# Performance work log

Hardware: AMD Instinct MI355X
Metric: run time of the kernel (lower is better)

## Reference

```python
import jax, jax.numpy as jnp
import numpy as np

N = 16384      # total nodes
SEQ = 512      # nodes per graph
NG = 32        # graphs (N = NG*SEQ)
D = 128        # dim_h
H = 8          # heads
E = 262144     # edges
BN_EPS = 1e-5


def _bn(x, g, b):
    # BatchNorm1d, training-mode stats over the node axis (biased var, as torch)
    mu = x.mean(axis=0)
    var = x.var(axis=0)
    return (x - mu) * jax.lax.rsqrt(var + BN_EPS) * g + b


def setup_inputs() -> dict:
    key = jax.random.key(0)
    ks = jax.random.split(key, 24)
    w = lambda k, shp: (jax.random.normal(k, shp, jnp.float32) * 0.05)
    x = jax.random.normal(ks[0], (N, D), jnp.float32)
    # within-graph edges: dst in same graph as src
    src = jax.random.randint(ks[1], (E,), 0, N, dtype=jnp.int32)
    dst = (src // SEQ) * SEQ + jax.random.randint(ks[2], (E,), 0, SEQ, dtype=jnp.int32)
    edge_index = jnp.stack([src, dst])
    edge_attr = jax.random.normal(ks[3], (E, D), jnp.float32)
    return {
        'x': x, 'edge_index': edge_index, 'edge_attr': edge_attr,
        'gin_w1': w(ks[4], (D, D)), 'gin_b1': jnp.zeros((D,), jnp.float32),
        'gin_w2': w(ks[5], (D, D)), 'gin_b2': jnp.zeros((D,), jnp.float32),
        'bn1l_g': jnp.ones((D,), jnp.float32), 'bn1l_b': jnp.zeros((D,), jnp.float32),
        'in_proj_w': w(ks[6], (3 * D, D)), 'in_proj_b': jnp.zeros((3 * D,), jnp.float32),
        'out_proj_w': w(ks[7], (D, D)), 'out_proj_b': jnp.zeros((D,), jnp.float32),
        'bn1a_g': jnp.ones((D,), jnp.float32), 'bn1a_b': jnp.zeros((D,), jnp.float32),
        'ff_w1': w(ks[8], (D, 2 * D)), 'ff_b1': jnp.zeros((2 * D,), jnp.float32),
        'ff_w2': w(ks[9], (2 * D, D)), 'ff_b2': jnp.zeros((D,), jnp.float32),
        'bn2_g': jnp.ones((D,), jnp.float32), 'bn2_b': jnp.zeros((D,), jnp.float32),
    }


def reference(x, edge_index, edge_attr, gin_w1, gin_b1, gin_w2, gin_b2,
              bn1l_g, bn1l_b, in_proj_w, in_proj_b, out_proj_w, out_proj_b,
              bn1a_g, bn1a_b, ff_w1, ff_b1, ff_w2, ff_b2, bn2_g, bn2_b):
    h_in1 = x
    src, dst = edge_index[0], edge_index[1]
    # --- local GINE: aggr_i = sum_{j->i} relu(x_j + e_ji); nn((1+eps)*x + aggr), eps=0
    msg = jax.nn.relu(x[src] + edge_attr)                 # [E, D]
    aggr = jax.ops.segment_sum(msg, dst, num_segments=N)  # [N, D]
    z = x + aggr
    h_local = jax.nn.relu(z @ gin_w1 + gin_b1) @ gin_w2 + gin_b2
    h_local = h_in1 + h_local                # residual (dropout=0)
    h_local = _bn(h_local, bn1l_g, bn1l_b)
    # --- global Transformer attention over dense batch (equal-size graphs => reshape)
    hd = x.reshape(NG, SEQ, D)
    qkv = hd @ in_proj_w.T + in_proj_b       # [NG, SEQ, 3D]
    q, k, v = jnp.split(qkv, 3, axis=-1)
    dh = D // H
    q = q.reshape(NG, SEQ, H, dh)
    k = k.reshape(NG, SEQ, H, dh)
    v = v.reshape(NG, SEQ, H, dh)
    scores = jnp.einsum('bqhd,bkhd->bhqk', q, k) / jnp.sqrt(jnp.float32(dh))
    attn = jax.nn.softmax(scores, axis=-1)
    o = jnp.einsum('bhqk,bkhd->bqhd', attn, v).reshape(NG, SEQ, D)
    h_attn = (o @ out_proj_w.T + out_proj_b).reshape(N, D)
    h_attn = h_in1 + h_attn                  # residual (attn_dropout=0)
    h_attn = _bn(h_attn, bn1a_g, bn1a_b)
    # --- combine + FFN block
    h = h_local + h_attn
    ff = jax.nn.relu(h @ ff_w1 + ff_b1) @ ff_w2 + ff_b2
    h = h + ff
    h = _bn(h, bn2_g, bn2_b)
    return h
```

## Files before the change

kernel.cpp:

```cpp
#include <hip/hip_runtime.h>


#define N_NODES 16384
#define SEQL    512
#define NGRAPH  32
#define DIM     128
#define NHEAD   8
#define DHEAD   16
#define NEDGE   262144

typedef __bf16 bf16;
typedef __bf16 bf16x8 __attribute__((ext_vector_type(8)));
typedef __bf16 bf16x4 __attribute__((ext_vector_type(4)));
typedef float  f32x4  __attribute__((ext_vector_type(4)));

__device__ inline f32x4 mfma16(bf16x8 a, bf16x8 b, f32x4 c) {
  return __builtin_amdgcn_mfma_f32_16x16x32_bf16(a, b, c, 0, 0, 0);
}

__global__ __launch_bounds__(256) void prep_k(
    const float* __restrict__ gw1, const float* __restrict__ gw2,
    const float* __restrict__ ipw, const float* __restrict__ opw,
    const float* __restrict__ fw1, const float* __restrict__ fw2,
    bf16* __restrict__ W, int* __restrict__ cnt, float* __restrict__ stats)
{
  int i = blockIdx.x * 256 + threadIdx.x;
  if (i < 16384) {
    W[i] = (bf16)gw1[(i & 127) * 128 + (i >> 7)];
  } else if (i < 32768) {
    int j = i - 16384;
    W[i] = (bf16)gw2[(j & 127) * 128 + (j >> 7)];
  } else if (i < 81920) {
    W[i] = (bf16)ipw[i - 32768];
  } else if (i < 98304) {
    W[i] = (bf16)opw[i - 81920];
  } else if (i < 131072) {
    int j = i - 98304;
    W[i] = (bf16)fw1[(j & 127) * 256 + (j >> 7)];
  } else if (i < 163840) {
    int j = i - 131072;
    W[i] = (bf16)fw2[(j & 255) * 128 + (j >> 8)];
  } else if (i < 163840 + 16384) {
    cnt[i - 163840] = 0;
  } else if (i < 163840 + 16384 + 768) {
    stats[i - 163840 - 16384] = 0.f;
  }
}

__global__ __launch_bounds__(256) void edge_count_k(const int* __restrict__ ei,
                                                    int* __restrict__ cnt)
{
  int e = blockIdx.x * 256 + threadIdx.x;
  if (e < NEDGE) atomicAdd(&cnt[ei[NEDGE + e]], 1);
}

__global__ __launch_bounds__(1024) void scan_k(const int* __restrict__ cnt,
                                               int* __restrict__ off,
                                               int* __restrict__ cur)
{
  __shared__ int part[1024];
  int t = threadIdx.x;
  int base = t * 16;
  int v[16];
  int s = 0;
#pragma unroll
  for (int j = 0; j < 16; ++j) { v[j] = s; s += cnt[base + j]; }
  part[t] = s;
  __syncthreads();
  for (int d = 1; d < 1024; d <<= 1) {
    int y = (t >= d) ? part[t - d] : 0;
    __syncthreads();
    part[t] += y;
    __syncthreads();
  }
  int bo = (t > 0) ? part[t - 1] : 0;
#pragma unroll
  for (int j = 0; j < 16; ++j) {
    int o = bo + v[j];
    off[base + j] = o;
    cur[base + j] = o;
  }
  if (t == 1023) off[16384] = bo + s;
}

__global__ __launch_bounds__(256) void edge_scatter_k(const int* __restrict__ ei,
                                                      int* __restrict__ cur,
                                                      int2* __restrict__ se)
{
  int e = blockIdx.x * 256 + threadIdx.x;
  if (e < NEDGE) {
    int s = ei[e];
    int d = ei[NEDGE + e];
    int p = atomicAdd(&cur[d], 1);
    se[p] = make_int2(s, e);
  }
}

__global__ __launch_bounds__(256) void aggr_k(
    const float* __restrict__ x, const float* __restrict__ ea,
    const int* __restrict__ off, const int2* __restrict__ se,
    float* __restrict__ z)
{
  int node = blockIdx.x * 4 + (threadIdx.x >> 6);
  int lane = threadIdx.x & 63;
  int c = lane * 2;
  int o0 = off[node], o1 = off[node + 1];
  float a0 = 0.f, a1 = 0.f;
  int j = o0;
  for (; j + 4 <= o1; j += 4) {
    int2 p0 = se[j], p1 = se[j + 1], p2 = se[j + 2], p3 = se[j + 3];
    float2 x0 = *(const float2*)(x + (size_t)p0.x * 128 + c);
    float2 e0 = *(const float2*)(ea + (size_t)p0.y * 128 + c);
    float2 x1 = *(const float2*)(x + (size_t)p1.x * 128 + c);
    float2 e1 = *(const float2*)(ea + (size_t)p1.y * 128 + c);
    float2 x2 = *(const float2*)(x + (size_t)p2.x * 128 + c);
    float2 e2 = *(const float2*)(ea + (size_t)p2.y * 128 + c);
    float2 x3 = *(const float2*)(x + (size_t)p3.x * 128 + c);
    float2 e3 = *(const float2*)(ea + (size_t)p3.y * 128 + c);
    a0 += fmaxf(x0.x + e0.x, 0.f) + fmaxf(x1.x + e1.x, 0.f) +
          fmaxf(x2.x + e2.x, 0.f) + fmaxf(x3.x + e3.x, 0.f);
    a1 += fmaxf(x0.y + e0.y, 0.f) + fmaxf(x1.y + e1.y, 0.f) +
          fmaxf(x2.y + e2.y, 0.f) + fmaxf(x3.y + e3.y, 0.f);
  }
  for (; j < o1; ++j) {
    int2 p = se[j];
    float2 xe = *(const float2*)(x + (size_t)p.x * 128 + c);
    float2 ae = *(const float2*)(ea + (size_t)p.y * 128 + c);
    a0 += fmaxf(xe.x + ae.x, 0.f);
    a1 += fmaxf(xe.y + ae.y, 0.f);
  }
  float2 xn = *(const float2*)(x + (size_t)node * 128 + c);
  *(float2*)(z + (size_t)node * 128 + c) = make_float2(xn.x + a0, xn.y + a1);
}

template <int NCH, int KCH, bool RELU, int RESID, bool STATS, int OUTMODE>
__global__ __launch_bounds__(256) void gemm_k(
    const float* __restrict__ Aptr, const bf16* __restrict__ Wt,
    const float* __restrict__ bias, const float* __restrict__ resid,
    float* __restrict__ outF, bf16* __restrict__ oq, bf16* __restrict__ okk,
    bf16* __restrict__ ov, float* __restrict__ stats)
{
  constexpr int KIN = KCH * 128;
  constexpr int NLD = NCH * 128;
  __shared__ bf16 Alds[32][136];
  __shared__ bf16 Wlds[128][136];
  __shared__ float slds[256];
  int tid = threadIdx.x;
  int wave = tid >> 6, lane = tid & 63, quad = lane >> 4, l16 = lane & 15;
  int rg = wave >> 1, chalf = wave & 1;
  int m0 = blockIdx.x * 32;
  if (STATS) slds[tid] = 0.f;

  for (int nc = 0; nc < NCH; ++nc) {
    f32x4 acc[4];
#pragma unroll
    for (int t = 0; t < 4; ++t) acc[t] = (f32x4){0.f, 0.f, 0.f, 0.f};
    for (int kc = 0; kc < KCH; ++kc) {
      if (!(nc == 0 && kc == 0)) __syncthreads();
      if (nc == 0 || KCH > 1) {
        int r = tid >> 3, c16 = (tid & 7) * 16;
        const float* src = Aptr + (size_t)(m0 + r) * KIN + kc * 128 + c16;
        float4 v0 = *(const float4*)(src);
        float4 v1 = *(const float4*)(src + 4);
        float4 v2 = *(const float4*)(src + 8);
        float4 v3 = *(const float4*)(src + 12);
        *(bf16x8*)&Alds[r][c16] =
            (bf16x8){(bf16)v0.x, (bf16)v0.y, (bf16)v0.z, (bf16)v0.w,
                     (bf16)v1.x, (bf16)v1.y, (bf16)v1.z, (bf16)v1.w};
        *(bf16x8*)&Alds[r][c16 + 8] =
            (bf16x8){(bf16)v2.x, (bf16)v2.y, (bf16)v2.z, (bf16)v2.w,
                     (bf16)v3.x, (bf16)v3.y, (bf16)v3.z, (bf16)v3.w};
      }
      {
        int n = tid >> 1, ch = (tid & 1) * 64;
        const bf16* src = Wt + (size_t)(nc * 128 + n) * KIN + kc * 128 + ch;
        bf16* dst = &Wlds[n][ch];
#pragma unroll
        for (int j = 0; j < 8; ++j)
          *(bf16x8*)(dst + j * 8) = *(const bf16x8*)(src + j * 8);
      }
      __syncthreads();
#pragma unroll
      for (int kt = 0; kt < 4; ++kt) {
        bf16x8 af = *(const bf16x8*)&Alds[rg * 16 + l16][kt * 32 + quad * 8];
#pragma unroll
        for (int nt = 0; nt < 4; ++nt) {
          bf16x8 bfr =
              *(const bf16x8*)&Wlds[chalf * 64 + nt * 16 + l16][kt * 32 + quad * 8];
          acc[nt] = mfma16(af, bfr, acc[nt]);
        }
      }
    }
    int rowb = m0 + rg * 16 + quad * 4;
#pragma unroll
    for (int nt = 0; nt < 4; ++nt) {
      int n = chalf * 64 + nt * 16 + l16;
      int gcol = nc * 128 + n;
      float bv = bias[gcol];
      float vals[4];
#pragma unroll
      for (int r = 0; r < 4; ++r) {
        float v = acc[nt][r] + bv;
        if (RELU) v = fmaxf(v, 0.f);
        if (RESID) v += resid[(size_t)(rowb + r) * 128 + n];
        vals[r] = v;
        if (OUTMODE == 0) {
          outF[(size_t)(rowb + r) * NLD + gcol] = v;
        } else {
          bf16* ob = (nc == 0) ? oq : ((nc == 1) ? okk : ov);
          ob[(size_t)(rowb + r) * 128 + n] = (bf16)v;
        }
      }
      if (STATS) {
        float s = vals[0] + vals[1] + vals[2] + vals[3];
        float q2 = vals[0] * vals[0] + vals[1] * vals[1] +
                   vals[2] * vals[2] + vals[3] * vals[3];
        s += __shfl_xor(s, 16);  s += __shfl_xor(s, 32);
        q2 += __shfl_xor(q2, 16); q2 += __shfl_xor(q2, 32);
        if (quad == 0) {
          atomicAdd(&slds[n * 2], s);
          atomicAdd(&slds[n * 2 + 1], q2);
        }
      }
    }
  }
  if (STATS) {
    __syncthreads();
    if (tid < 128) {
      atomicAdd(&stats[tid], slds[tid * 2]);
      atomicAdd(&stats[128 + tid], slds[tid * 2 + 1]);
    }
  }
}

__global__ __launch_bounds__(256) void attn_k(
    const bf16* __restrict__ qg, const bf16* __restrict__ kg,
    const bf16* __restrict__ vg, float* __restrict__ og)
{
  __shared__ bf16 Klds[512][16];
  __shared__ bf16 Vlds[16][520];
  __shared__ bf16 Plds[4][16][136];
  int b = blockIdx.x;
  int half = b & 1, hh = (b >> 1) & 7, g = b >> 4;
  int tid = threadIdx.x;
  const size_t gbase = (size_t)g * 512 * 128 + hh * 16;
  for (int r = tid; r < 512; r += 256) {
    const bf16* src = kg + gbase + (size_t)r * 128;
    *(bf16x8*)&Klds[r][0] = *(const bf16x8*)src;
    *(bf16x8*)&Klds[r][8] = *(const bf16x8*)(src + 8);
  }
  for (int r = tid; r < 512; r += 256) {
    const bf16* src = vg + gbase + (size_t)r * 128;
#pragma unroll
    for (int d = 0; d < 16; ++d) Vlds[d][r] = src[d];
  }
  __syncthreads();
  int wave = tid >> 6, lane = tid & 63, quad = lane >> 4, l16 = lane & 15;
  const bf16x8 z8 = {};
  for (int it = 0; it < 4; ++it) {
    int qt = half * 16 + it * 4 + wave;
    bf16x8 qf = z8;
    if (quad < 2)
      qf = *(const bf16x8*)(qg + gbase + (size_t)(qt * 16 + l16) * 128 + quad * 8);
    f32x4 S[32];
#pragma unroll
    for (int jt = 0; jt < 32; ++jt) {
      bf16x8 kf = z8;
      if (quad < 2) kf = *(const bf16x8*)&Klds[jt * 16 + l16][quad * 8];
      S[jt] = mfma16(kf, qf, (f32x4){0.f, 0.f, 0.f, 0.f});
    }
    float mx = -1e30f;
#pragma unroll
    for (int jt = 0; jt < 32; ++jt)
#pragma unroll
      for (int r = 0; r < 4; ++r) mx = fmaxf(mx, S[jt][r]);
    mx = fmaxf(mx, __shfl_xor(mx, 16));
    mx = fmaxf(mx, __shfl_xor(mx, 32));
    float sm = 0.f;
#pragma unroll
    for (int jt = 0; jt < 32; ++jt)
#pragma unroll
      for (int r = 0; r < 4; ++r) {
        float e = __expf((S[jt][r] - mx) * 0.25f);
        S[jt][r] = e;
        sm += e;
      }
    sm += __shfl_xor(sm, 16);
    sm += __shfl_xor(sm, 32);
    float rinv = 1.f / sm;
    f32x4 O = (f32x4){0.f, 0.f, 0.f, 0.f};
#pragma unroll
    for (int qd = 0; qd < 4; ++qd) {
#pragma unroll
      for (int jt2 = 0; jt2 < 8; ++jt2)
#pragma unroll
        for (int r = 0; r < 4; ++r)
          Plds[wave][l16][jt2 * 16 + quad * 4 + r] =
              (bf16)(S[qd * 8 + jt2][r] * rinv);
#pragma unroll
      for (int kt = 0; kt < 4; ++kt) {
        bf16x8 pf = *(const bf16x8*)&Plds[wave][l16][kt * 32 + quad * 8];
        bf16x8 vf = *(const bf16x8*)&Vlds[l16][qd * 128 + kt * 32 + quad * 8];
        O = mfma16(vf, pf, O);
      }
    }
    *(float4*)(og + (size_t)(g * 512 + qt * 16 + l16) * 128 + hh * 16 + quad * 4) =
        make_float4(O[0], O[1], O[2], O[3]);
  }
}

__global__ __launch_bounds__(256) void combine_k(
    const float* __restrict__ hl, const float* __restrict__ ha,
    const float* __restrict__ stats,
    const float* __restrict__ g1, const float* __restrict__ b1,
    const float* __restrict__ g2, const float* __restrict__ b2,
    float* __restrict__ h)
{
  __shared__ float sc1[128], sh1[128], sc2[128], sh2[128];
  int tid = threadIdx.x;
  if (tid < 128) {
    const float inv = 1.f / 16384.f;
    float mu = stats[tid] * inv;
    float var = stats[128 + tid] * inv - mu * mu;
    float s = g1[tid] * rsqrtf(var + 1e-5f);
    sc1[tid] = s; sh1[tid] = b1[tid] - mu * s;
    mu = stats[256 + tid] * inv;
    var = stats[384 + tid] * inv - mu * mu;
    s = g2[tid] * rsqrtf(var + 1e-5f);
    sc2[tid] = s; sh2[tid] = b2[tid] - mu * s;
  }
  __syncthreads();
  size_t i = ((size_t)blockIdx.x * 256 + tid) * 4;
  int c = (int)(i & 127);
  float4 a = *(const float4*)(hl + i);
  float4 bb = *(const float4*)(ha + i);
  float4 o;
  o.x = a.x * sc1[c] + sh1[c] + bb.x * sc2[c] + sh2[c];
  o.y = a.y * sc1[c + 1] + sh1[c + 1] + bb.y * sc2[c + 1] + sh2[c + 1];
  o.z = a.z * sc1[c + 2] + sh1[c + 2] + bb.z * sc2[c + 2] + sh2[c + 2];
  o.w = a.w * sc1[c + 3] + sh1[c + 3] + bb.w * sc2[c + 3] + sh2[c + 3];
  *(float4*)(h + i) = o;
}

__global__ __launch_bounds__(256) void apply_k(
    const float* __restrict__ h2, const float* __restrict__ stats,
    const float* __restrict__ g, const float* __restrict__ b,
    float* __restrict__ out)
{
  __shared__ float sc[128], sh[128];
  int tid = threadIdx.x;
  if (tid < 128) {
    const float inv = 1.f / 16384.f;
    float mu = stats[512 + tid] * inv;
    float var = stats[640 + tid] * inv - mu * mu;
    float s = g[tid] * rsqrtf(var + 1e-5f);
    sc[tid] = s; sh[tid] = b[tid] - mu * s;
  }
  __syncthreads();
  size_t i = ((size_t)blockIdx.x * 256 + tid) * 4;
  int c = (int)(i & 127);
  float4 a = *(const float4*)(h2 + i);
  float4 o;
  o.x = a.x * sc[c] + sh[c];
  o.y = a.y * sc[c + 1] + sh[c + 1];
  o.z = a.z * sc[c + 2] + sh[c + 2];
  o.w = a.w * sc[c + 3] + sh[c + 3];
  *(float4*)(out + i) = o;
}

extern "C" void kernel_launch(void* const* d_in, const int* in_sizes, int n_in,
                              void* d_out, int out_size, void* d_ws, size_t ws_size,
                              hipStream_t stream)
{
  (void)in_sizes; (void)n_in; (void)out_size; (void)ws_size;
  const float* x      = (const float*)d_in[0];
  const int*   ei     = (const int*)d_in[1];
  const float* ea     = (const float*)d_in[2];
  const float* gw1    = (const float*)d_in[3];
  const float* gb1    = (const float*)d_in[4];
  const float* gw2    = (const float*)d_in[5];
  const float* gb2    = (const float*)d_in[6];
  const float* bn1l_g = (const float*)d_in[7];
  const float* bn1l_b = (const float*)d_in[8];
  const float* ipw    = (const float*)d_in[9];
  const float* ipb    = (const float*)d_in[10];
  const float* opw    = (const float*)d_in[11];
  const float* opb    = (const float*)d_in[12];
  const float* bn1a_g = (const float*)d_in[13];
  const float* bn1a_b = (const float*)d_in[14];
  const float* fw1    = (const float*)d_in[15];
  const float* fb1    = (const float*)d_in[16];
  const float* fw2    = (const float*)d_in[17];
  const float* fb2    = (const float*)d_in[18];
  const float* bn2_g  = (const float*)d_in[19];
  const float* bn2_b  = (const float*)d_in[20];

  char* ws = (char*)d_ws;
  const size_t KB = 1024, MB = 1048576;
  bf16*  W     = (bf16*)(ws + 0);
  float* stats = (float*)(ws + 320 * KB);
  int*   cnt   = (int*)(ws + 384 * KB);
  int*   off   = (int*)(ws + 448 * KB);
  int*   cur   = (int*)(ws + 576 * KB);
  int2*  se    = (int2*)(ws + 640 * KB);
  float* z   = (float*)(ws + 3 * MB);
  float* hl  = (float*)(ws + 11 * MB);
  bf16*  qb  = (bf16*)(ws + 19 * MB);
  bf16*  kb  = (bf16*)(ws + 23 * MB);
  bf16*  vb  = (bf16*)(ws + 27 * MB);
  float* ob  = (float*)(ws + 31 * MB);
  float* ha  = (float*)(ws + 39 * MB);
  float* hb  = (float*)(ws + 47 * MB);
  float* t1  = (float*)qb;
  float* ff1 = z;
  float* h2  = ob;
  float* out = (float*)d_out;

  prep_k<<<708, 256, 0, stream>>>(gw1, gw2, ipw, opw, fw1, fw2, W, cnt, stats);
  edge_count_k<<<1024, 256, 0, stream>>>(ei, cnt);
  scan_k<<<1, 1024, 0, stream>>>(cnt, off, cur);
  edge_scatter_k<<<1024, 256, 0, stream>>>(ei, cur, se);
  aggr_k<<<4096, 256, 0, stream>>>(x, ea, off, se, z);
  gemm_k<1, 1, true, 0, false, 0><<<512, 256, 0, stream>>>(
      z, W + 0, gb1, nullptr, t1, nullptr, nullptr, nullptr, nullptr);
  gemm_k<1, 1, false, 1, true, 0><<<512, 256, 0, stream>>>(
      t1, W + 16384, gb2, x, hl, nullptr, nullptr, nullptr, stats + 0);
  gemm_k<3, 1, false, 0, false, 1><<<512, 256, 0, stream>>>(
      x, W + 32768, ipb, nullptr, nullptr, qb, kb, vb, nullptr);
  attn_k<<<512, 256, 0, stream>>>(qb, kb, vb, ob);
  gemm_k<1, 1, false, 1, true, 0><<<512, 256, 0, stream>>>(
      ob, W + 81920, opb, x, ha, nullptr, nullptr, nullptr, stats + 256);
  combine_k<<<2048, 256, 0, stream>>>(hl, ha, stats, bn1l_g, bn1l_b, bn1a_g, bn1a_b, hb);
  gemm_k<2, 1, true, 0, false, 0><<<512, 256, 0, stream>>>(
      hb, W + 98304, fb1, nullptr, ff1, nullptr, nullptr, nullptr, nullptr);
  gemm_k<1, 2, false, 1, true, 0><<<512, 256, 0, stream>>>(
      ff1, W + 131072, fb2, hb, h2, nullptr, nullptr, nullptr, stats + 512);
  apply_k<<<2048, 256, 0, stream>>>(h2, stats, bn2_g, bn2_b, out);
}
```

Before: 428.8 us.

## Fuse entire pipeline into one cooperative persistent megakernel with grid syncs

Replaces the chain of separate launches (weight prep, edge count, scan, scatter, aggregation, GEMMs, attention, BN combine, apply) with a single cooperative kernel that uses grid.sync between phases. The two GIN GEMMs and the QKV projection are fused per row tile, keeping intermediates in shared memory, and the scan is parallelised across blocks. The aim is to remove launch overhead and intermediate global round-trips. In exchange it adds grid-wide barriers, caps occupancy at the cooperative grid size, and puts heavy pressure on shared memory.

```diff
diff --git a/kernel.cpp b/kernel.cpp
--- a/kernel.cpp
+++ b/kernel.cpp
@@ -1,371 +1,494 @@
 #include <hip/hip_runtime.h>
-
-
-#define N_NODES 16384
-#define SEQL    512
-#define NGRAPH  32
-#define DIM     128
-#define NHEAD   8
-#define DHEAD   16
-#define NEDGE   262144
+#include <hip/hip_cooperative_groups.h>
+
+namespace cg = cooperative_groups;
+
+
+#define NNODES 16384
+#define NEDGE  262144
 
 typedef __bf16 bf16;
 typedef __bf16 bf16x8 __attribute__((ext_vector_type(8)));
-typedef __bf16 bf16x4 __attribute__((ext_vector_type(4)));
 typedef float  f32x4  __attribute__((ext_vector_type(4)));
 
 __device__ inline f32x4 mfma16(bf16x8 a, bf16x8 b, f32x4 c) {
   return __builtin_amdgcn_mfma_f32_16x16x32_bf16(a, b, c, 0, 0, 0);
 }
 
-__global__ __launch_bounds__(256) void prep_k(
-    const float* __restrict__ gw1, const float* __restrict__ gw2,
-    const float* __restrict__ ipw, const float* __restrict__ opw,
-    const float* __restrict__ fw1, const float* __restrict__ fw2,
-    bf16* __restrict__ W, int* __restrict__ cnt, float* __restrict__ stats)
-{
-  int i = blockIdx.x * 256 + threadIdx.x;
-  if (i < 16384) {
-    W[i] = (bf16)gw1[(i & 127) * 128 + (i >> 7)];
-  } else if (i < 32768) {
-    int j = i - 16384;
-    W[i] = (bf16)gw2[(j & 127) * 128 + (j >> 7)];
-  } else if (i < 81920) {
-    W[i] = (bf16)ipw[i - 32768];
-  } else if (i < 98304) {
-    W[i] = (bf16)opw[i - 81920];
-  } else if (i < 131072) {
-    int j = i - 98304;
-    W[i] = (bf16)fw1[(j & 127) * 256 + (j >> 7)];
-  } else if (i < 163840) {
-    int j = i - 131072;
-    W[i] = (bf16)fw2[(j & 255) * 128 + (j >> 8)];
-  } else if (i < 163840 + 16384) {
-    cnt[i - 163840] = 0;
-  } else if (i < 163840 + 16384 + 768) {
-    stats[i - 163840 - 16384] = 0.f;
-  }
+struct PK {
+  const float *x, *ea; const int* ei;
+  const float *gw1, *gb1, *gw2, *gb2;
+  const float *bn1l_g, *bn1l_b;
+  const float *ipw, *ipb, *opw, *opb;
+  const float *bn1a_g, *bn1a_b;
+  const float *fw1, *fb1, *fw2, *fb2;
+  const float *bn2_g, *bn2_b;
+  bf16* W; float* stats; int *cnt, *off, *cur, *psum; int2* se;
+  float *z, *hl, *ob, *ha, *h2, *out;
+  bf16 *qb, *kb, *vb;
+};
+
+#define SMEM_BYTES 79872
+
+__device__ inline void load_w(const bf16* __restrict__ src, int ks,
+                              bf16* __restrict__ Wl, int tid) {
+  int n = tid >> 1, c = (tid & 1) * 64;
+  const bf16* s = src + (size_t)n * ks + c;
+  bf16* d = Wl + n * 136 + c;
+#pragma unroll
+  for (int j = 0; j < 8; ++j)
+    *(bf16x8*)(d + j * 8) = *(const bf16x8*)(s + j * 8);
 }
 
-__global__ __launch_bounds__(256) void edge_count_k(const int* __restrict__ ei,
-                                                    int* __restrict__ cnt)
-{
-  int e = blockIdx.x * 256 + threadIdx.x;
-  if (e < NEDGE) atomicAdd(&cnt[ei[NEDGE + e]], 1);
+__device__ inline void load_a32(const float* __restrict__ src,
+                                bf16* __restrict__ Al, int tid) {
+  int r = tid >> 3, c = (tid & 7) * 16;
+  const float* s = src + (size_t)r * 128 + c;
+  float4 v0 = *(const float4*)s, v1 = *(const float4*)(s + 4);
+  float4 v2 = *(const float4*)(s + 8), v3 = *(const float4*)(s + 12);
+  *(bf16x8*)(Al + r * 136 + c) =
+      (bf16x8){(bf16)v0.x, (bf16)v0.y, (bf16)v0.z, (bf16)v0.w,
+               (bf16)v1.x, (bf16)v1.y, (bf16)v1.z, (bf16)v1.w};
+  *(bf16x8*)(Al + r * 136 + c + 8) =
+      (bf16x8){(bf16)v2.x, (bf16)v2.y, (bf16)v2.z, (bf16)v2.w,
+               (bf16)v3.x, (bf16)v3.y, (bf16)v3.z, (bf16)v3.w};
 }
 
-__global__ __launch_bounds__(1024) void scan_k(const int* __restrict__ cnt,
-                                               int* __restrict__ off,
-                                               int* __restrict__ cur)
-{
-  __shared__ int part[1024];
-  int t = threadIdx.x;
-  int base = t * 16;
-  int v[16];
-  int s = 0;
-#pragma unroll
-  for (int j = 0; j < 16; ++j) { v[j] = s; s += cnt[base + j]; }
-  part[t] = s;
-  __syncthreads();
-  for (int d = 1; d < 1024; d <<= 1) {
-    int y = (t >= d) ? part[t - d] : 0;
-    __syncthreads();
-    part[t] += y;
-    __syncthreads();
-  }
-  int bo = (t > 0) ? part[t - 1] : 0;
-#pragma unroll
-  for (int j = 0; j < 16; ++j) {
-    int o = bo + v[j];
-    off[base + j] = o;
-    cur[base + j] = o;
-  }
-  if (t == 1023) off[16384] = bo + s;
+__device__ inline void do_gemm(const bf16* __restrict__ A, int lda,
+                               const bf16* __restrict__ Wl,
+                               int rg, int chalf, int quad, int l16,
+                               f32x4 acc[4]) {
+#pragma unroll
+  for (int kt = 0; kt < 4; ++kt) {
+    bf16x8 af = *(const bf16x8*)(A + (rg * 16 + l16) * lda + kt * 32 + quad * 8);
+#pragma unroll
+    for (int nt = 0; nt < 4; ++nt) {
+      bf16x8 bfr = *(const bf16x8*)(Wl + (chalf * 64 + nt * 16 + l16) * 136 +
+                                    kt * 32 + quad * 8);
+      acc[nt] = mfma16(af, bfr, acc[nt]);
+    }
+  }
 }
 
-__global__ __launch_bounds__(256) void edge_scatter_k(const int* __restrict__ ei,
-                                                      int* __restrict__ cur,
-                                                      int2* __restrict__ se)
-{
-  int e = blockIdx.x * 256 + threadIdx.x;
-  if (e < NEDGE) {
-    int s = ei[e];
-    int d = ei[NEDGE + e];
-    int p = atomicAdd(&cur[d], 1);
-    se[p] = make_int2(s, e);
-  }
-}
-
-__global__ __launch_bounds__(256) void aggr_k(
-    const float* __restrict__ x, const float* __restrict__ ea,
-    const int* __restrict__ off, const int2* __restrict__ se,
-    float* __restrict__ z)
-{
-  int node = blockIdx.x * 4 + (threadIdx.x >> 6);
-  int lane = threadIdx.x & 63;
-  int c = lane * 2;
-  int o0 = off[node], o1 = off[node + 1];
-  float a0 = 0.f, a1 = 0.f;
-  int j = o0;
-  for (; j + 4 <= o1; j += 4) {
-    int2 p0 = se[j], p1 = se[j + 1], p2 = se[j + 2], p3 = se[j + 3];
-    float2 x0 = *(const float2*)(x + (size_t)p0.x * 128 + c);
-    float2 e0 = *(const float2*)(ea + (size_t)p0.y * 128 + c);
-    float2 x1 = *(const float2*)(x + (size_t)p1.x * 128 + c);
-    float2 e1 = *(const float2*)(ea + (size_t)p1.y * 128 + c);
-    float2 x2 = *(const float2*)(x + (size_t)p2.x * 128 + c);
-    float2 e2 = *(const float2*)(ea + (size_t)p2.y * 128 + c);
-    float2 x3 = *(const float2*)(x + (size_t)p3.x * 128 + c);
-    float2 e3 = *(const float2*)(ea + (size_t)p3.y * 128 + c);
-    a0 += fmaxf(x0.x + e0.x, 0.f) + fmaxf(x1.x + e1.x, 0.f) +
-          fmaxf(x2.x + e2.x, 0.f) + fmaxf(x3.x + e3.x, 0.f);
-    a1 += fmaxf(x0.y + e0.y, 0.f) + fmaxf(x1.y + e1.y, 0.f) +
-          fmaxf(x2.y + e2.y, 0.f) + fmaxf(x3.y + e3.y, 0.f);
-  }
-  for (; j < o1; ++j) {
-    int2 p = se[j];
-    float2 xe = *(const float2*)(x + (size_t)p.x * 128 + c);
-    float2 ae = *(const float2*)(ea + (size_t)p.y * 128 + c);
-    a0 += fmaxf(xe.x + ae.x, 0.f);
-    a1 += fmaxf(xe.y + ae.y, 0.f);
-  }
-  float2 xn = *(const float2*)(x + (size_t)node * 128 + c);
-  *(float2*)(z + (size_t)node * 128 + c) = make_float2(xn.x + a0, xn.y + a1);
-}
-
-template <int NCH, int KCH, bool RELU, int RESID, bool STATS, int OUTMODE>
-__global__ __launch_bounds__(256) void gemm_k(
-    const float* __restrict__ Aptr, const bf16* __restrict__ Wt,
-    const float* __restrict__ bias, const float* __restrict__ resid,
-    float* __restrict__ outF, bf16* __restrict__ oq, bf16* __restrict__ okk,
-    bf16* __restrict__ ov, float* __restrict__ stats)
-{
-  constexpr int KIN = KCH * 128;
-  constexpr int NLD = NCH * 128;
-  __shared__ bf16 Alds[32][136];
-  __shared__ bf16 Wlds[128][136];
-  __shared__ float slds[256];
-  int tid = threadIdx.x;
-  int wave = tid >> 6, lane = tid & 63, quad = lane >> 4, l16 = lane & 15;
-  int rg = wave >> 1, chalf = wave & 1;
-  int m0 = blockIdx.x * 32;
-  if (STATS) slds[tid] = 0.f;
-
-  for (int nc = 0; nc < NCH; ++nc) {
+__global__ __launch_bounds__(256, 2) void mega_k(PK p) {
+  cg::grid_group grid = cg::this_grid();
+  __shared__ __align__(16) char smem[SMEM_BYTES];
+  bf16*  Abf  = (bf16*)smem;
+  bf16*  Wl   = (bf16*)(smem + 8704);
+  float* slds = (float*)(smem + 43520);
+  bf16*  Tt   = (bf16*)(smem + 44544);
+  float* hbt  = (float*)(smem + 61440);
+  float* bnc  = (float*)(smem + 77824);
+  bf16*  Klds = (bf16*)smem;
+  bf16*  Vlds = (bf16*)(smem + 16384);
+  bf16*  Plds = (bf16*)(smem + 33024);
+  int*   ilds = (int*)smem;
+
+  const int tid = threadIdx.x, bid = blockIdx.x, nb = gridDim.x;
+  const int wave = tid >> 6, lane = tid & 63, quad = lane >> 4, l16 = lane & 15;
+  const int rg = wave >> 1, chalf = wave & 1;
+  const int gsz = nb * 256;
+
+  for (int i = bid * 256 + tid; i < 163840 + 16384 + 768; i += gsz) {
+    if (i < 16384) {
+      p.W[i] = (bf16)p.gw1[(i & 127) * 128 + (i >> 7)];
+    } else if (i < 32768) {
+      int j = i - 16384;
+      p.W[i] = (bf16)p.gw2[(j & 127) * 128 + (j >> 7)];
+    } else if (i < 81920) {
+      p.W[i] = (bf16)p.ipw[i - 32768];
+    } else if (i < 98304) {
+      p.W[i] = (bf16)p.opw[i - 81920];
+    } else if (i < 131072) {
+      int j = i - 98304;
+      p.W[i] = (bf16)p.fw1[(j & 127) * 256 + (j >> 7)];
+    } else if (i < 163840) {
+      int j = i - 131072;
+      p.W[i] = (bf16)p.fw2[(j & 255) * 128 + (j >> 8)];
+    } else if (i < 163840 + 16384) {
+      p.cnt[i - 163840] = 0;
+    } else {
+      p.stats[i - 163840 - 16384] = 0.f;
+    }
+  }
+  grid.sync();
+  for (int e = bid * 256 + tid; e < NEDGE; e += gsz)
+    atomicAdd(&p.cnt[p.ei[NEDGE + e]], 1);
+  grid.sync();
+  for (int c = bid; c < 512; c += nb) {
+    if (wave == 0) {
+      int v = (lane < 32) ? p.cnt[c * 32 + lane] : 0;
+      int xv = v;
+#pragma unroll
+      for (int d = 1; d < 32; d <<= 1) {
+        int u = __shfl_up(xv, d, 64);
+        if (lane >= d) xv += u;
+      }
+      if (lane < 32) p.off[c * 32 + lane] = xv - v;
+      if (lane == 31) p.psum[c] = xv;
+    }
+  }
+  grid.sync();
+  if (bid == 0) {
+    int a = p.psum[2 * tid], b2 = p.psum[2 * tid + 1];
+    ilds[tid] = a + b2;
+    __syncthreads();
+    for (int d = 1; d < 256; d <<= 1) {
+      int y = (tid >= d) ? ilds[tid - d] : 0;
+      __syncthreads();
+      ilds[tid] += y;
+      __syncthreads();
+    }
+    int base = (tid > 0) ? ilds[tid - 1] : 0;
+    p.psum[2 * tid] = base;
+    p.psum[2 * tid + 1] = base + a;
+    if (tid == 255) p.off[16384] = ilds[255];
+  }
+  grid.sync();
+  for (int i = bid * 256 + tid; i < 16384; i += gsz) {
+    int o = p.off[i] + p.psum[i >> 5];
+    p.off[i] = o;
+    p.cur[i] = o;
+  }
+  grid.sync();
+  for (int e = bid * 256 + tid; e < NEDGE; e += gsz) {
+    int s = p.ei[e], d = p.ei[NEDGE + e];
+    int pos = atomicAdd(&p.cur[d], 1);
+    p.se[pos] = make_int2(s, e);
+  }
+  grid.sync();
+  {
+    int c2 = lane * 2;
+    int nw = nb * 4;
+    for (int node = bid * 4 + wave; node < NNODES; node += nw) {
+      int o0 = p.off[node], o1 = p.off[node + 1];
+      float a0 = 0.f, a1 = 0.f;
+      int j = o0;
+      for (; j + 4 <= o1; j += 4) {
+        int2 q0 = p.se[j], q1 = p.se[j + 1], q2 = p.se[j + 2], q3 = p.se[j + 3];
+        float2 x0 = *(const float2*)(p.x + (size_t)q0.x * 128 + c2);
+        float2 e0 = *(const float2*)(p.ea + (size_t)q0.y * 128 + c2);
+        float2 x1 = *(const float2*)(p.x + (size_t)q1.x * 128 + c2);
+        float2 e1 = *(const float2*)(p.ea + (size_t)q1.y * 128 + c2);
+        float2 x2 = *(const float2*)(p.x + (size_t)q2.x * 128 + c2);
+        float2 e2 = *(const float2*)(p.ea + (size_t)q2.y * 128 + c2);
+        float2 x3 = *(const float2*)(p.x + (size_t)q3.x * 128 + c2);
+        float2 e3 = *(const float2*)(p.ea + (size_t)q3.y * 128 + c2);
+        a0 += fmaxf(x0.x + e0.x, 0.f) + fmaxf(x1.x + e1.x, 0.f) +
+              fmaxf(x2.x + e2.x, 0.f) + fmaxf(x3.x + e3.x, 0.f);
+        a1 += fmaxf(x0.y + e0.y, 0.f) + fmaxf(x1.y + e1.y, 0.f) +
+              fmaxf(x2.y + e2.y, 0.f) + fmaxf(x3.y + e3.y, 0.f);
+      }
+      for (; j < o1; ++j) {
+        int2 q = p.se[j];
+        float2 xe = *(const float2*)(p.x + (size_t)q.x * 128 + c2);
+        float2 ae = *(const float2*)(p.ea + (size_t)q.y * 128 + c2);
+        a0 += fmaxf(xe.x + ae.x, 0.f);
+        a1 += fmaxf(xe.y + ae.y, 0.f);
+      }
+      float2 xn = *(const float2*)(p.x + (size_t)node * 128 + c2);
+      *(float2*)(p.z + (size_t)node * 128 + c2) =
+          make_float2(xn.x + a0, xn.y + a1);
+    }
+  }
+  grid.sync();
+  for (int ch = bid; ch < 512; ch += nb) {
+    int m0 = ch * 32;
+    int rowb = m0 + rg * 16 + quad * 4;
+    slds[tid] = 0.f;
+    load_a32(p.z + (size_t)m0 * 128, Abf, tid);
+    load_w(p.W, 128, Wl, tid);
+    __syncthreads();
     f32x4 acc[4];
 #pragma unroll
     for (int t = 0; t < 4; ++t) acc[t] = (f32x4){0.f, 0.f, 0.f, 0.f};
-    for (int kc = 0; kc < KCH; ++kc) {
-      if (!(nc == 0 && kc == 0)) __syncthreads();
-      if (nc == 0 || KCH > 1) {
-        int r = tid >> 3, c16 = (tid & 7) * 16;
-        const float* src = Aptr + (size_t)(m0 + r) * KIN + kc * 128 + c16;
-        float4 v0 = *(const float4*)(src);
-        float4 v1 = *(const float4*)(src + 4);
-        float4 v2 = *(const float4*)(src + 8);
-        float4 v3 = *(const float4*)(src + 12);
-        *(bf16x8*)&Alds[r][c16] =
-            (bf16x8){(bf16)v0.x, (bf16)v0.y, (bf16)v0.z, (bf16)v0.w,
-                     (bf16)v1.x, (bf16)v1.y, (bf16)v1.z, (bf16)v1.w};
-        *(bf16x8*)&Alds[r][c16 + 8] =
-            (bf16x8){(bf16)v2.x, (bf16)v2.y, (bf16)v2.z, (bf16)v2.w,
-                     (bf16)v3.x, (bf16)v3.y, (bf16)v3.z, (bf16)v3.w};
-      }
-      {
-        int n = tid >> 1, ch = (tid & 1) * 64;
-        const bf16* src = Wt + (size_t)(nc * 128 + n) * KIN + kc * 128 + ch;
-        bf16* dst = &Wlds[n][ch];
-#pragma unroll
-        for (int j = 0; j < 8; ++j)
-          *(bf16x8*)(dst + j * 8) = *(const bf16x8*)(src + j * 8);
-      }
-      __syncthreads();
-#pragma unroll
-      for (int kt = 0; kt < 4; ++kt) {
-        bf16x8 af = *(const bf16x8*)&Alds[rg * 16 + l16][kt * 32 + quad * 8];
-#pragma unroll
-        for (int nt = 0; nt < 4; ++nt) {
-          bf16x8 bfr =
-              *(const bf16x8*)&Wlds[chalf * 64 + nt * 16 + l16][kt * 32 + quad * 8];
-          acc[nt] = mfma16(af, bfr, acc[nt]);
+    do_gemm(Abf, 136, Wl, rg, chalf, quad, l16, acc);
+#pragma unroll
+    for (int nt = 0; nt < 4; ++nt) {
+      int col = chalf * 64 + nt * 16 + l16;
+      float bv = p.gb1[col];
+#pragma unroll
+      for (int r = 0; r < 4; ++r) {
+        float v = fmaxf(acc[nt][r] + bv, 0.f);
+        Tt[(rg * 16 + quad * 4 + r) * 136 + col] = (bf16)v;
+      }
+    }
+    __syncthreads();
+    load_w(p.W + 16384, 128, Wl, tid);
+    __syncthreads();
+#pragma unroll
+    for (int t = 0; t < 4; ++t) acc[t] = (f32x4){0.f, 0.f, 0.f, 0.f};
+    do_gemm(Tt, 136, Wl, rg, chalf, quad, l16, acc);
+#pragma unroll
+    for (int nt = 0; nt < 4; ++nt) {
+      int col = chalf * 64 + nt * 16 + l16;
+      float bv = p.gb2[col];
+      float vals[4];
+#pragma unroll
+      for (int r = 0; r < 4; ++r) {
+        float v = acc[nt][r] + bv + p.x[(size_t)(rowb + r) * 128 + col];
+        vals[r] = v;
+        p.hl[(size_t)(rowb + r) * 128 + col] = v;
+      }
+      float s = vals[0] + vals[1] + vals[2] + vals[3];
+      float q2 = vals[0] * vals[0] + vals[1] * vals[1] +
+                 vals[2] * vals[2] + vals[3] * vals[3];
+      s += __shfl_xor(s, 16); s += __shfl_xor(s, 32);
+      q2 += __shfl_xor(q2, 16); q2 += __shfl_xor(q2, 32);
+      if (quad == 0) {
+        atomicAdd(&slds[col * 2], s);
+        atomicAdd(&slds[col * 2 + 1], q2);
+      }
+    }
+    __syncthreads();
+    if (tid < 128) {
+      atomicAdd(&p.stats[tid], slds[tid * 2]);
+      atomicAdd(&p.stats[128 + tid], slds[tid * 2 + 1]);
+    }
+    load_a32(p.x + (size_t)m0 * 128, Abf, tid);
+    for (int nc = 0; nc < 3; ++nc) {
+      load_w(p.W + 32768 + nc * 16384, 128, Wl, tid);
+      __syncthreads();
+#pragma unroll
+      for (int t = 0; t < 4; ++t) acc[t] = (f32x4){0.f, 0.f, 0.f, 0.f};
+      do_gemm(Abf, 136, Wl, rg, chalf, quad, l16, acc);
+      bf16* dst = (nc == 0) ? p.qb : ((nc == 1) ? p.kb : p.vb);
+#pragma unroll
+      for (int nt = 0; nt < 4; ++nt) {
+        int col = chalf * 64 + nt * 16 + l16;
+        float bv = p.ipb[nc * 128 + col];
+#pragma unroll
+        for (int r = 0; r < 4; ++r)
+          dst[(size_t)(rowb + r) * 128 + col] = (bf16)(acc[nt][r] + bv);
+      }
+      __syncthreads();
+    }
+  }
+  grid.sync();
+  for (int t6 = bid; t6 < 512; t6 += nb) {
+    int half = t6 & 1, hh = (t6 >> 1) & 7, g = t6 >> 4;
+    const size_t gbase = (size_t)g * 512 * 128 + hh * 16;
+    for (int r = tid; r < 512; r += 256) {
+      const bf16* src = p.kb + gbase + (size_t)r * 128;
+      *(bf16x8*)&Klds[r * 16] = *(const bf16x8*)src;
+      *(bf16x8*)&Klds[r * 16 + 8] = *(const bf16x8*)(src + 8);
+    }
+    for (int r = tid; r < 512; r += 256) {
+      const bf16* src = p.vb + gbase + (size_t)r * 128;
+#pragma unroll
+      for (int d = 0; d < 16; ++d) Vlds[d * 520 + r] = src[d];
+    }
+    __syncthreads();
+    const bf16x8 z8 = {};
+    for (int it = 0; it < 4; ++it) {
+      int qt = half * 16 + it * 4 + wave;
+      bf16x8 qf = z8;
+      if (quad < 2)
+        qf = *(const bf16x8*)(p.qb + gbase + (size_t)(qt * 16 + l16) * 128 +
+                              quad * 8);
+      f32x4 S[32];
+#pragma unroll
+      for (int jt = 0; jt < 32; ++jt) {
+        bf16x8 kf = z8;
+        if (quad < 2) kf = *(const bf16x8*)&Klds[(jt * 16 + l16) * 16 + quad * 8];
+        S[jt] = mfma16(kf, qf, (f32x4){0.f, 0.f, 0.f, 0.f});
+      }
+      float mx = -1e30f;
+#pragma unroll
+      for (int jt = 0; jt < 32; ++jt)
+#pragma unroll
+        for (int r = 0; r < 4; ++r) mx = fmaxf(mx, S[jt][r]);
+      mx = fmaxf(mx, __shfl_xor(mx, 16));
+      mx = fmaxf(mx, __shfl_xor(mx, 32));
+      float sm = 0.f;
+#pragma unroll
+      for (int jt = 0; jt < 32; ++jt)
+#pragma unroll
+        for (int r = 0; r < 4; ++r) {
+          float e = __expf((S[jt][r] - mx) * 0.25f);
+          S[jt][r] = e;
+          sm += e;
         }
-      }
-    }
+      sm += __shfl_xor(sm, 16);
+      sm += __shfl_xor(sm, 32);
+      float rinv = 1.f / sm;
+      f32x4 O = (f32x4){0.f, 0.f, 0.f, 0.f};
+#pragma unroll
+      for (int qd = 0; qd < 4; ++qd) {
+#pragma unroll
+        for (int jt2 = 0; jt2 < 8; ++jt2)
+#pragma unroll
+          for (int r = 0; r < 4; ++r)
+            Plds[(wave * 16 + l16) * 136 + jt2 * 16 + quad * 4 + r] =
+                (bf16)(S[qd * 8 + jt2][r] * rinv);
+#pragma unroll
+        for (int kt = 0; kt < 4; ++kt) {
+          bf16x8 pf = *(const bf16x8*)&Plds[(wave * 16 + l16) * 136 + kt * 32 +
+                                            quad * 8];
+          bf16x8 vf = *(const bf16x8*)&Vlds[l16 * 520 + qd * 128 + kt * 32 +
+                                            quad * 8];
+          O = mfma16(vf, pf, O);
+        }
+      }
+      *(float4*)(p.ob + (size_t)(g * 512 + qt * 16 + l16) * 128 + hh * 16 +
+                 quad * 4) = make_float4(O[0], O[1], O[2], O[3]);
+    }
+    __syncthreads();
+  }
+  grid.sync();
+  for (int ch = bid; ch < 512; ch += nb) {
+    int m0 = ch * 32;
     int rowb = m0 + rg * 16 + quad * 4;
+    slds[tid] = 0.f;
+    load_a32(p.ob + (size_t)m0 * 128, Abf, tid);
+    load_w(p.W + 81920, 128, Wl, tid);
+    __syncthreads();
+    f32x4 acc[4];
+#pragma unroll
+    for (int t = 0; t < 4; ++t) acc[t] = (f32x4){0.f, 0.f, 0.f, 0.f};
+    do_gemm(Abf, 136, Wl, rg, chalf, quad, l16, acc);
 #pragma unroll
     for (int nt = 0; nt < 4; ++nt) {
-      int n = chalf * 64 + nt * 16 + l16;
-      int gcol = nc * 128 + n;
-      float bv = bias[gcol];
+      int col = chalf * 64 + nt * 16 + l16;
+      float bv = p.opb[col];
       float vals[4];
 #pragma unroll
       for (int r = 0; r < 4; ++r) {
-        float v = acc[nt][r] + bv;
-        if (RELU) v = fmaxf(v, 0.f);
-        if (RESID) v += resid[(size_t)(rowb + r) * 128 + n];
+        float v = acc[nt][r] + bv + p.x[(size_t)(rowb + r) * 128 + col];
         vals[r] = v;
-        if (OUTMODE == 0) {
-          outF[(size_t)(rowb + r) * NLD + gcol] = v;
-        } else {
-          bf16* ob = (nc == 0) ? oq : ((nc == 1) ? okk : ov);
-          ob[(size_t)(rowb + r) * 128 + n] = (bf16)v;
+        p.ha[(size_t)(rowb + r) * 128 + col] = v;
+      }
+      float s = vals[0] + vals[1] + vals[2] + vals[3];
+      float q2 = vals[0] * vals[0] + vals[1] * vals[1] +
+                 vals[2] * vals[2] + vals[3] * vals[3];
+      s += __shfl_xor(s, 16); s += __shfl_xor(s, 32);
+      q2 += __shfl_xor(q2, 16); q2 += __shfl_xor(q2, 32);
+      if (quad == 0) {
+        atomicAdd(&slds[col * 2], s);
+        atomicAdd(&slds[col * 2 + 1], q2);
+      }
+    }
+    __syncthreads();
+    if (tid < 128) {
+      atomicAdd(&p.stats[256 + tid], slds[tid * 2]);
+      atomicAdd(&p.stats[384 + tid], slds[tid * 2 + 1]);
+    }
+    __syncthreads();
+  }
+  grid.sync();
+  for (int ch = bid; ch < 512; ch += nb) {
+    int m0 = ch * 32;
+    int rowb = m0 + rg * 16 + quad * 4;
+    if (tid < 128) {
+      const float inv = 1.f / 16384.f;
+      float mu = p.stats[tid] * inv;
+      float var = p.stats[128 + tid] * inv - mu * mu;
+      float s = p.bn1l_g[tid] * rsqrtf(var + 1e-5f);
+      bnc[tid] = s;
+      bnc[128 + tid] = p.bn1l_b[tid] - mu * s;
+      mu = p.stats[256 + tid] * inv;
+      var = p.stats[384 + tid] * inv - mu * mu;
+      s = p.bn1a_g[tid] * rsqrtf(var + 1e-5f);
+      bnc[256 + tid] = s;
+      bnc[384 + tid] = p.bn1a_b[tid] - mu * s;
+    }
+    slds[tid] = 0.f;
+    __syncthreads();
+    {
+      int r = tid >> 3, c16 = (tid & 7) * 16;
+#pragma unroll
+      for (int j = 0; j < 4; ++j) {
+        int c = c16 + j * 4;
+        float4 a = *(const float4*)(p.hl + (size_t)(m0 + r) * 128 + c);
+        float4 b = *(const float4*)(p.ha + (size_t)(m0 + r) * 128 + c);
+        float4 o;
+        o.x = a.x * bnc[c] + bnc[128 + c] + b.x * bnc[256 + c] + bnc[384 + c];
+        o.y = a.y * bnc[c + 1] + bnc[129 + c] + b.y * bnc[257 + c] + bnc[385 + c];
+        o.z = a.z * bnc[c + 2] + bnc[130 + c] + b.z * bnc[258 + c] + bnc[386 + c];
+        o.w = a.w * bnc[c + 3] + bnc[131 + c] + b.w * bnc[259 + c] + bnc[387 + c];
+        *(float4*)(hbt + r * 128 + c) = o;
+        Abf[r * 136 + c] = (bf16)o.x;
+        Abf[r * 136 + c + 1] = (bf16)o.y;
+        Abf[r * 136 + c + 2] = (bf16)o.z;
+        Abf[r * 136 + c + 3] = (bf16)o.w;
+      }
+    }
+    f32x4 acc[4];
+    for (int nc = 0; nc < 2; ++nc) {
+      load_w(p.W + 98304 + nc * 16384, 128, Wl, tid);
+      __syncthreads();
+#pragma unroll
+      for (int t = 0; t < 4; ++t) acc[t] = (f32x4){0.f, 0.f, 0.f, 0.f};
+      do_gemm(Abf, 136, Wl, rg, chalf, quad, l16, acc);
+#pragma unroll
+      for (int nt = 0; nt < 4; ++nt) {
+        int col = chalf * 64 + nt * 16 + l16;
+        float bv = p.fb1[nc * 128 + col];
+#pragma unroll
+        for (int r = 0; r < 4; ++r) {
+          float v = fmaxf(acc[nt][r] + bv, 0.f);
+          Tt[(rg * 16 + quad * 4 + r) * 264 + nc * 128 + col] = (bf16)v;
         }
       }
-      if (STATS) {
-        float s = vals[0] + vals[1] + vals[2] + vals[3];
-        float q2 = vals[0] * vals[0] + vals[1] * vals[1] +
-                   vals[2] * vals[2] + vals[3] * vals[3];
-        s += __shfl_xor(s, 16);  s += __shfl_xor(s, 32);
-        q2 += __shfl_xor(q2, 16); q2 += __shfl_xor(q2, 32);
-        if (quad == 0) {
-          atomicAdd(&slds[n * 2], s);
-          atomicAdd(&slds[n * 2 + 1], q2);
-        }
-      }
-    }
-  }
-  if (STATS) {
+      __syncthreads();
+    }
+    f32x4 acc2[4];
+#pragma unroll
+    for (int t = 0; t < 4; ++t) acc2[t] = (f32x4){0.f, 0.f, 0.f, 0.f};
+    for (int kc = 0; kc < 2; ++kc) {
+      load_w(p.W + 131072 + kc * 128, 256, Wl, tid);
+      __syncthreads();
+      do_gemm(Tt + kc * 128, 264, Wl, rg, chalf, quad, l16, acc2);
+      __syncthreads();
+    }
+#pragma unroll
+    for (int nt = 0; nt < 4; ++nt) {
+      int col = chalf * 64 + nt * 16 + l16;
+      float bv = p.fb2[col];
+      float vals[4];
+#pragma unroll
+      for (int r = 0; r < 4; ++r) {
+        float v = acc2[nt][r] + bv + hbt[(rg * 16 + quad * 4 + r) * 128 + col];
+        vals[r] = v;
+        p.h2[(size_t)(rowb + r) * 128 + col] = v;
+      }
+      float s = vals[0] + vals[1] + vals[2] + vals[3];
+      float q2 = vals[0] * vals[0] + vals[1] * vals[1] +
+                 vals[2] * vals[2] + vals[3] * vals[3];
+      s += __shfl_xor(s, 16); s += __shfl_xor(s, 32);
+      q2 += __shfl_xor(q2, 16); q2 += __shfl_xor(q2, 32);
+      if (quad == 0) {
+        atomicAdd(&slds[col * 2], s);
+        atomicAdd(&slds[col * 2 + 1], q2);
+      }
+    }
     __syncthreads();
     if (tid < 128) {
-      atomicAdd(&stats[tid], slds[tid * 2]);
-      atomicAdd(&stats[128 + tid], slds[tid * 2 + 1]);
-    }
-  }
-}
-
-__global__ __launch_bounds__(256) void attn_k(
-    const bf16* __restrict__ qg, const bf16* __restrict__ kg,
-    const bf16* __restrict__ vg, float* __restrict__ og)
-{
-  __shared__ bf16 Klds[512][16];
-  __shared__ bf16 Vlds[16][520];
-  __shared__ bf16 Plds[4][16][136];
-  int b = blockIdx.x;
-  int half = b & 1, hh = (b >> 1) & 7, g = b >> 4;
-  int tid = threadIdx.x;
-  const size_t gbase = (size_t)g * 512 * 128 + hh * 16;
-  for (int r = tid; r < 512; r += 256) {
-    const bf16* src = kg + gbase + (size_t)r * 128;
-    *(bf16x8*)&Klds[r][0] = *(const bf16x8*)src;
-    *(bf16x8*)&Klds[r][8] = *(const bf16x8*)(src + 8);
-  }
-  for (int r = tid; r < 512; r += 256) {
-    const bf16* src = vg + gbase + (size_t)r * 128;
-#pragma unroll
-    for (int d = 0; d < 16; ++d) Vlds[d][r] = src[d];
-  }
-  __syncthreads();
-  int wave = tid >> 6, lane = tid & 63, quad = lane >> 4, l16 = lane & 15;
-  const bf16x8 z8 = {};
-  for (int it = 0; it < 4; ++it) {
-    int qt = half * 16 + it * 4 + wave;
-    bf16x8 qf = z8;
-    if (quad < 2)
-      qf = *(const bf16x8*)(qg + gbase + (size_t)(qt * 16 + l16) * 128 + quad * 8);
-    f32x4 S[32];
-#pragma unroll
-    for (int jt = 0; jt < 32; ++jt) {
-      bf16x8 kf = z8;
-      if (quad < 2) kf = *(const bf16x8*)&Klds[jt * 16 + l16][quad * 8];
-      S[jt] = mfma16(kf, qf, (f32x4){0.f, 0.f, 0.f, 0.f});
-    }
-    float mx = -1e30f;
-#pragma unroll
-    for (int jt = 0; jt < 32; ++jt)
-#pragma unroll
-      for (int r = 0; r < 4; ++r) mx = fmaxf(mx, S[jt][r]);
-    mx = fmaxf(mx, __shfl_xor(mx, 16));
-    mx = fmaxf(mx, __shfl_xor(mx, 32));
-    float sm = 0.f;
-#pragma unroll
-    for (int jt = 0; jt < 32; ++jt)
-#pragma unroll
-      for (int r = 0; r < 4; ++r) {
-        float e = __expf((S[jt][r] - mx) * 0.25f);
-        S[jt][r] = e;
-        sm += e;
-      }
-    sm += __shfl_xor(sm, 16);
-    sm += __shfl_xor(sm, 32);
-    float rinv = 1.f / sm;
-    f32x4 O = (f32x4){0.f, 0.f, 0.f, 0.f};
-#pragma unroll
-    for (int qd = 0; qd < 4; ++qd) {
-#pragma unroll
-      for (int jt2 = 0; jt2 < 8; ++jt2)
-#pragma unroll
-        for (int r = 0; r < 4; ++r)
-          Plds[wave][l16][jt2 * 16 + quad * 4 + r] =
-              (bf16)(S[qd * 8 + jt2][r] * rinv);
-#pragma unroll
-      for (int kt = 0; kt < 4; ++kt) {
-        bf16x8 pf = *(const bf16x8*)&Plds[wave][l16][kt * 32 + quad * 8];
-        bf16x8 vf = *(const bf16x8*)&Vlds[l16][qd * 128 + kt * 32 + quad * 8];
-        O = mfma16(vf, pf, O);
-      }
-    }
-    *(float4*)(og + (size_t)(g * 512 + qt * 16 + l16) * 128 + hh * 16 + quad * 4) =
-        make_float4(O[0], O[1], O[2], O[3]);
-  }
-}
-
-__global__ __launch_bounds__(256) void combine_k(
-    const float* __restrict__ hl, const float* __restrict__ ha,
-    const float* __restrict__ stats,
-    const float* __restrict__ g1, const float* __restrict__ b1,
-    const float* __restrict__ g2, const float* __restrict__ b2,
-    float* __restrict__ h)
-{
-  __shared__ float sc1[128], sh1[128], sc2[128], sh2[128];
-  int tid = threadIdx.x;
+      atomicAdd(&p.stats[512 + tid], slds[tid * 2]);
+      atomicAdd(&p.stats[640 + tid], slds[tid * 2 + 1]);
+    }
+    __syncthreads();
+  }
+  grid.sync();
   if (tid < 128) {
     const float inv = 1.f / 16384.f;
-    float mu = stats[tid] * inv;
-    float var = stats[128 + tid] * inv - mu * mu;
-    float s = g1[tid] * rsqrtf(var + 1e-5f);
-    sc1[tid] = s; sh1[tid] = b1[tid] - mu * s;
-    mu = stats[256 + tid] * inv;
-    var = stats[384 + tid] * inv - mu * mu;
-    s = g2[tid] * rsqrtf(var + 1e-5f);
-    sc2[tid] = s; sh2[tid] = b2[tid] - mu * s;
+    float mu = p.stats[512 + tid] * inv;
+    float var = p.stats[640 + tid] * inv - mu * mu;
+    float s = p.bn2_g[tid] * rsqrtf(var + 1e-5f);
+    bnc[tid] = s;
+    bnc[128 + tid] = p.bn2_b[tid] - mu * s;
   }
   __syncthreads();
-  size_t i = ((size_t)blockIdx.x * 256 + tid) * 4;
-  int c = (int)(i & 127);
-  float4 a = *(const float4*)(hl + i);
-  float4 bb = *(const float4*)(ha + i);
-  float4 o;
-  o.x = a.x * sc1[c] + sh1[c] + bb.x * sc2[c] + sh2[c];
-  o.y = a.y * sc1[c + 1] + sh1[c + 1] + bb.y * sc2[c + 1] + sh2[c + 1];
-  o.z = a.z * sc1[c + 2] + sh1[c + 2] + bb.z * sc2[c + 2] + sh2[c + 2];
-  o.w = a.w * sc1[c + 3] + sh1[c + 3] + bb.w * sc2[c + 3] + sh2[c + 3];
-  *(float4*)(h + i) = o;
-}
-
-__global__ __launch_bounds__(256) void apply_k(
-    const float* __restrict__ h2, const float* __restrict__ stats,
-    const float* __restrict__ g, const float* __restrict__ b,
-    float* __restrict__ out)
-{
-  __shared__ float sc[128], sh[128];
-  int tid = threadIdx.x;
-  if (tid < 128) {
-    const float inv = 1.f / 16384.f;
-    float mu = stats[512 + tid] * inv;
-    float var = stats[640 + tid] * inv - mu * mu;
-    float s = g[tid] * rsqrtf(var + 1e-5f);
-    sc[tid] = s; sh[tid] = b[tid] - mu * s;
-  }
-  __syncthreads();
-  size_t i = ((size_t)blockIdx.x * 256 + tid) * 4;
-  int c = (int)(i & 127);
-  float4 a = *(const float4*)(h2 + i);
-  float4 o;
-  o.x = a.x * sc[c] + sh[c];
-  o.y = a.y * sc[c + 1] + sh[c + 1];
-  o.z = a.z * sc[c + 2] + sh[c + 2];
-  o.w = a.w * sc[c + 3] + sh[c + 3];
-  *(float4*)(out + i) = o;
+  for (int i = bid * 256 + tid; i < NNODES * 32; i += gsz) {
+    int c = (i & 31) * 4;
+    float4 a = ((const float4*)p.h2)[i];
+    float4 o;
+    o.x = a.x * bnc[c] + bnc[128 + c];
+    o.y = a.y * bnc[c + 1] + bnc[129 + c];
+    o.z = a.z * bnc[c + 2] + bnc[130 + c];
+    o.w = a.w * bnc[c + 3] + bnc[131 + c];
+    ((float4*)p.out)[i] = o;
+  }
 }
 
 extern "C" void kernel_launch(void* const* d_in, const int* in_sizes, int n_in,
@@ -373,67 +496,51 @@
                               hipStream_t stream)
 {
   (void)in_sizes; (void)n_in; (void)out_size; (void)ws_size;
-  const float* x      = (const float*)d_in[0];
-  const int*   ei     = (const int*)d_in[1];
-  const float* ea     = (const float*)d_in[2];
-  const float* gw1    = (const float*)d_in[3];
-  const float* gb1    = (const float*)d_in[4];
-  const float* gw2    = (const float*)d_in[5];
-  const float* gb2    = (const float*)d_in[6];
-  const float* bn1l_g = (const float*)d_in[7];
-  const float* bn1l_b = (const float*)d_in[8];
-  const float* ipw    = (const float*)d_in[9];
-  const float* ipb    = (const float*)d_in[10];
-  const float* opw    = (const float*)d_in[11];
-  const float* opb    = (const float*)d_in[12];
-  const float* bn1a_g = (const float*)d_in[13];
-  const float* bn1a_b = (const float*)d_in[14];
-  const float* fw1    = (const float*)d_in[15];
-  const float* fb1    = (const float*)d_in[16];
-  const float* fw2    = (const float*)d_in[17];
-  const float* fb2    = (const float*)d_in[18];
-  const float* bn2_g  = (const float*)d_in[19];
-  const float* bn2_b  = (const float*)d_in[20];
-
   char* ws = (char*)d_ws;
   const size_t KB = 1024, MB = 1048576;
-  bf16*  W     = (bf16*)(ws + 0);
-  float* stats = (float*)(ws + 320 * KB);
-  int*   cnt   = (int*)(ws + 384 * KB);
-  int*   off   = (int*)(ws + 448 * KB);
-  int*   cur   = (int*)(ws + 576 * KB);
-  int2*  se    = (int2*)(ws + 640 * KB);
-  float* z   = (float*)(ws + 3 * MB);
-  float* hl  = (float*)(ws + 11 * MB);
-  bf16*  qb  = (bf16*)(ws + 19 * MB);
-  bf16*  kb  = (bf16*)(ws + 23 * MB);
-  bf16*  vb  = (bf16*)(ws + 27 * MB);
-  float* ob  = (float*)(ws + 31 * MB);
-  float* ha  = (float*)(ws + 39 * MB);
-  float* hb  = (float*)(ws + 47 * MB);
-  float* t1  = (float*)qb;
-  float* ff1 = z;
-  float* h2  = ob;
-  float* out = (float*)d_out;
-
-  prep_k<<<708, 256, 0, stream>>>(gw1, gw2, ipw, opw, fw1, fw2, W, cnt, stats);
-  edge_count_k<<<1024, 256, 0, stream>>>(ei, cnt);
-  scan_k<<<1, 1024, 0, stream>>>(cnt, off, cur);
-  edge_scatter_k<<<1024, 256, 0, stream>>>(ei, cur, se);
-  aggr_k<<<4096, 256, 0, stream>>>(x, ea, off, se, z);
-  gemm_k<1, 1, true, 0, false, 0><<<512, 256, 0, stream>>>(
-      z, W + 0, gb1, nullptr, t1, nullptr, nullptr, nullptr, nullptr);
-  gemm_k<1, 1, false, 1, true, 0><<<512, 256, 0, stream>>>(
-      t1, W + 16384, gb2, x, hl, nullptr, nullptr, nullptr, stats + 0);
-  gemm_k<3, 1, false, 0, false, 1><<<512, 256, 0, stream>>>(
-      x, W + 32768, ipb, nullptr, nullptr, qb, kb, vb, nullptr);
-  attn_k<<<512, 256, 0, stream>>>(qb, kb, vb, ob);
-  gemm_k<1, 1, false, 1, true, 0><<<512, 256, 0, stream>>>(
-      ob, W + 81920, opb, x, ha, nullptr, nullptr, nullptr, stats + 256);
-  combine_k<<<2048, 256, 0, stream>>>(hl, ha, stats, bn1l_g, bn1l_b, bn1a_g, bn1a_b, hb);
-  gemm_k<2, 1, true, 0, false, 0><<<512, 256, 0, stream>>>(
-      hb, W + 98304, fb1, nullptr, ff1, nullptr, nullptr, nullptr, nullptr);
-  gemm_k<1, 2, false, 1, true, 0><<<512, 256, 0, stream>>>(
-      ff1, W + 131072, fb2, hb, h2, nullptr, nullptr, nullptr, stats + 512);
-  apply_k<<<2048, 256, 0, stream>>>(h2, stats, bn2_g, bn2_b, out);
+  PK p;
+  p.x      = (const float*)d_in[0];
+  p.ei     = (const int*)d_in[1];
+  p.ea     = (const float*)d_in[2];
+  p.gw1    = (const float*)d_in[3];
+  p.gb1    = (const float*)d_in[4];
+  p.gw2    = (const float*)d_in[5];
+  p.gb2    = (const float*)d_in[6];
+  p.bn1l_g = (const float*)d_in[7];
+  p.bn1l_b = (const float*)d_in[8];
+  p.ipw    = (const float*)d_in[9];
+  p.ipb    = (const float*)d_in[10];
+  p.opw    = (const float*)d_in[11];
+  p.opb    = (const float*)d_in[12];
+  p.bn1a_g = (const float*)d_in[13];
+  p.bn1a_b = (const float*)d_in[14];
+  p.fw1    = (const float*)d_in[15];
+  p.fb1    = (const float*)d_in[16];
+  p.fw2    = (const float*)d_in[17];
+  p.fb2    = (const float*)d_in[18];
+  p.bn2_g  = (const float*)d_in[19];
+  p.bn2_b  = (const float*)d_in[20];
+  p.W     = (bf16*)(ws + 0);
+  p.stats = (float*)(ws + 320 * KB);
+  p.cnt   = (int*)(ws + 384 * KB);
+  p.off   = (int*)(ws + 448 * KB);
+  p.psum  = (int*)(ws + 540 * KB);
+  p.cur   = (int*)(ws + 576 * KB);
+  p.se    = (int2*)(ws + 640 * KB);
+  p.z     = (float*)(ws + 3 * MB);
+  p.hl    = (float*)(ws + 11 * MB);
+  p.qb    = (bf16*)(ws + 19 * MB);
+  p.kb    = (bf16*)(ws + 23 * MB);
+  p.vb    = (bf16*)(ws + 27 * MB);
+  p.ob    = (float*)(ws + 31 * MB);
+  p.ha    = (float*)(ws + 39 * MB);
+  p.h2    = (float*)(ws + 47 * MB);
+  p.out   = (float*)d_out;
+
+  int maxb = 1;
+  (void)hipOccupancyMaxActiveBlocksPerMultiprocessor(&maxb, mega_k, 256, 0);
+  int grid = (maxb >= 2) ? 512 : 256;
+  void* args[] = { (void*)&p };
+  (void)hipLaunchCooperativeKernel((void*)mega_k, dim3(grid), dim3(256),
+                                   args, 0, stream);
 }
```

Result: slower. 792.5 us (+84.8%).
